# Kernel optimization log

Hardware: AMD Instinct MI355X
Metric: run time of the kernel (lower is better)

The kernel has to match this reference:

```python
import jax, jax.numpy as jnp
import numpy as np

B, S = 16, 1024
V, D, P = 100000, 256, 8


def setup_inputs() -> dict:
    key = jax.random.key(0)
    k1, k2, k3, k4 = jax.random.split(key, 4)
    x = jax.random.randint(k1, (B, S), 0, V, dtype=jnp.int64 if jax.config.jax_enable_x64 else jnp.int32)
    emb_table = jax.random.normal(k2, (V, D), dtype=jnp.float32)
    weight = jax.random.normal(k3, (P, D, D), dtype=jnp.float32)
    partitions = jax.random.randint(k4, (V,), 0, P, dtype=jnp.int32)
    return {"x": x, "emb_table": emb_table, "weight": weight, "partitions": partitions}


def reference(x, emb_table, weight, partitions):
    P_, Dz, Dx = weight.shape
    # mask[p, x] = 1 for x < D >> p (reset_parameters halves active dim per partition)
    active = (Dx >> jnp.arange(P_))  # [P]
    mask = (jnp.arange(Dx)[None, :] < active[:, None]).astype(weight.dtype)  # [P, Dx]
    mw = weight * mask[:, None, :]  # [P, Dz, Dx], masked partition weights

    emb = emb_table[x]          # [B, S, Dx] token embeddings
    part = partitions[x]        # [B, S] partition id per token

    # Compute all P candidate outputs (small fixed P), then select per token.
    # Mathematically identical to gathering mw[part] and doing per-token matvec,
    # but avoids the huge [B,S,Dz,Dx] gathered-weight intermediate.
    all_out = jnp.einsum('bsx,pzx->bspz', emb, mw)  # [B, S, P, Dz]
    out = jnp.take_along_axis(all_out, part[..., None, None], axis=2)[..., 0, :]  # [B, S, Dz]
    return out
```

## Files before the change

kernel.cpp:

```cpp
#include <hip/hip_runtime.h>

__global__ void bucket_k(const int* __restrict__ x, const int* __restrict__ parts,
                         int* __restrict__ counts, int* __restrict__ buckets, int NT) {
    __shared__ int lcount[8];
    __shared__ int lbase[8];
    const int tid = threadIdx.x;
    if (tid < 8) lcount[tid] = 0;
    __syncthreads();

    const int i = blockIdx.x * blockDim.x + tid;
    int p = 0, lpos = 0;
    const bool valid = (i < NT);
    if (valid) {
        p = parts[x[i]];
        lpos = atomicAdd(&lcount[p], 1);
    }
    __syncthreads();
    if (tid < 8)
        lbase[tid] = lcount[tid] ? atomicAdd(&counts[tid], lcount[tid]) : 0;
    __syncthreads();
    if (valid)
        buckets[(size_t)p * NT + lbase[p] + lpos] = i;
}

#define KC 32
#define XB 32

__global__ __launch_bounds__(256)
void fge_gemm(const int* __restrict__ x,
              const float* __restrict__ emb,
              const float* __restrict__ weight,
              const int* __restrict__ counts,
              const int* __restrict__ buckets,
              float* __restrict__ out, int NT) {
    const int p = blockIdx.z;
    const int n = counts[p];
    if ((int)(blockIdx.x * 64) >= n) return;
    const int z0  = blockIdx.y * 64;
    const int K   = 256 >> p;
    const int tid = threadIdx.x;

    __shared__ __align__(16) float w_lds[256][64];
    __shared__ __align__(16) float e_lds[KC][64];
    __shared__ int vrow[64];
    __shared__ int oidx[64];

    {
        const int Kpad = (K < KC) ? KC : K;
        const int wrow = tid >> 2;
        const float* wbase = weight + ((size_t)p * 256 + (z0 + wrow)) * 256;
        for (int colb = (tid & 3) * 4; colb < Kpad; colb += 16) {
            float4 v = *(const float4*)(wbase + colb);
            float vv[4] = {v.x, v.y, v.z, v.w};
#pragma unroll
            for (int c = 0; c < 4; ++c)
                w_lds[colb + c][wrow] = (colb + c < K) ? vv[c] : 0.f;
        }
    }

    const int tz  = tid & 15;
    const int tt  = tid >> 4;
    const int t_l = tid & 63;
    const int xh  = tid >> 6;
    const int nch = (K + KC - 1) / KC;

    for (int t0 = blockIdx.x * 64; t0 < n; t0 += XB * 64) {
        const int ntile = min(64, n - t0);

        __syncthreads();
        if (tid < 64) {
            int idx = 0, row = 0;
            if (t_l < ntile) {
                idx = buckets[(size_t)p * NT + t0 + t_l];
                row = x[idx];
            }
            oidx[t_l] = idx;
            vrow[t_l] = row;
        }
        __syncthreads();

        float acc[4][4] = {};

        for (int ch = 0; ch < nch; ++ch) {
            {
                const bool tv = (t_l < ntile);
                const float* er = emb + (size_t)vrow[t_l] * 256;
                const int gxb = ch * KC + xh * 8;
                float4 a = *(const float4*)(er + gxb);
                float4 b = *(const float4*)(er + gxb + 4);
                float va[8] = {a.x, a.y, a.z, a.w, b.x, b.y, b.z, b.w};
#pragma unroll
                for (int c = 0; c < 8; ++c) {
                    int gx = gxb + c;
                    e_lds[xh * 8 + c][t_l] = (tv && gx < K) ? va[c] : 0.f;
                }
            }
            __syncthreads();

#pragma unroll
            for (int c = 0; c < KC; ++c) {
                const float4 ev = *(const float4*)&e_lds[c][tt * 4];
                const float4 wv = *(const float4*)&w_lds[ch * KC + c][tz * 4];
                const float ea[4] = {ev.x, ev.y, ev.z, ev.w};
                const float wa[4] = {wv.x, wv.y, wv.z, wv.w};
#pragma unroll
                for (int i = 0; i < 4; ++i)
#pragma unroll
                    for (int j = 0; j < 4; ++j)
                        acc[i][j] = fmaf(ea[i], wa[j], acc[i][j]);
            }
            __syncthreads();
        }

#pragma unroll
        for (int i = 0; i < 4; ++i) {
            const int t = tt * 4 + i;
            if (t < ntile) {
                float4 o = {acc[i][0], acc[i][1], acc[i][2], acc[i][3]};
                *(float4*)(out + (size_t)oidx[t] * 256 + z0 + tz * 4) = o;
            }
        }
    }
}

__global__ void naive_k(const int* __restrict__ x, const float* __restrict__ emb,
                        const float* __restrict__ w, const int* __restrict__ parts,
                        float* __restrict__ out, int D, int P) {
    const int i = blockIdx.x;
    const int tokrow = x[i];
    const int p = parts[tokrow];
    const int K = D >> p;
    const float* er = emb + (size_t)tokrow * D;
    for (int z = threadIdx.x; z < D; z += blockDim.x) {
        const float* wr = w + ((size_t)p * D + z) * D;
        float acc = 0.f;
        for (int k = 0; k < K; ++k) acc = fmaf(er[k], wr[k], acc);
        out[(size_t)i * D + z] = acc;
    }
}

extern "C" void kernel_launch(void* const* d_in, const int* in_sizes, int n_in,
                              void* d_out, int out_size, void* d_ws, size_t ws_size,
                              hipStream_t stream) {
    const int*   xi    = (const int*)d_in[0];
    const float* emb   = (const float*)d_in[1];
    const float* wgt   = (const float*)d_in[2];
    const int*   parts = (const int*)d_in[3];
    float* out = (float*)d_out;

    const int NT = in_sizes[0];
    const long long V = in_sizes[3];
    const int D = (int)(in_sizes[1] / V);
    const int P = (int)(in_sizes[2] / ((long long)D * D));
    const size_t need = 32 + (size_t)P * (size_t)NT * sizeof(int);

    if (D == 256 && P == 8 && ws_size >= need) {
        int* counts  = (int*)d_ws;
        int* buckets = (int*)((char*)d_ws + 32);
        hipMemsetAsync(counts, 0, 32, stream);
        bucket_k<<<(NT + 255) / 256, 256, 0, stream>>>(xi, parts, counts, buckets, NT);
        dim3 grid(XB, 4, 8);
        fge_gemm<<<grid, 256, 0, stream>>>(xi, emb, wgt, counts, buckets, out, NT);
    } else {
        naive_k<<<NT, 256, 0, stream>>>(xi, emb, wgt, parts, out, D, P);
    }
}
```

Before: 162.6 us.

## Fuse partition bucketing into GEMM with per-block local token compaction

Removes the separate bucketing kernel, the memset and the global bucket workspace. Each block now scans a fixed range of 384 tokens, keeps those belonging to its partition in shared-memory lists, and runs the tiled matvec on them. This cuts two launches and a global scatter pass. The cost is that every block rescans x and parts for its range, and the grid grows to 43×4×8 blocks that each load a weight slab of up to 64 KB even when they hold only about 48 tokens.

```diff
diff --git a/kernel.cpp b/kernel.cpp
--- a/kernel.cpp
+++ b/kernel.cpp
@@ -1,49 +1,40 @@
 #include <hip/hip_runtime.h>
 
-__global__ void bucket_k(const int* __restrict__ x, const int* __restrict__ parts,
-                         int* __restrict__ counts, int* __restrict__ buckets, int NT) {
-    __shared__ int lcount[8];
-    __shared__ int lbase[8];
-    const int tid = threadIdx.x;
-    if (tid < 8) lcount[tid] = 0;
-    __syncthreads();
-
-    const int i = blockIdx.x * blockDim.x + tid;
-    int p = 0, lpos = 0;
-    const bool valid = (i < NT);
-    if (valid) {
-        p = parts[x[i]];
-        lpos = atomicAdd(&lcount[p], 1);
-    }
-    __syncthreads();
-    if (tid < 8)
-        lbase[tid] = lcount[tid] ? atomicAdd(&counts[tid], lcount[tid]) : 0;
-    __syncthreads();
-    if (valid)
-        buckets[(size_t)p * NT + lbase[p] + lpos] = i;
-}
-
 #define KC 32
-#define XB 32
+#define RANGE 384
 
 __global__ __launch_bounds__(256)
-void fge_gemm(const int* __restrict__ x,
-              const float* __restrict__ emb,
-              const float* __restrict__ weight,
-              const int* __restrict__ counts,
-              const int* __restrict__ buckets,
-              float* __restrict__ out, int NT) {
-    const int p = blockIdx.z;
-    const int n = counts[p];
-    if ((int)(blockIdx.x * 64) >= n) return;
+void fge_fused(const int* __restrict__ x,
+               const float* __restrict__ emb,
+               const float* __restrict__ weight,
+               const int* __restrict__ parts,
+               float* __restrict__ out, int NT) {
+    const int p   = blockIdx.z;
     const int z0  = blockIdx.y * 64;
+    const int s0  = blockIdx.x * RANGE;
+    if (s0 >= NT) return;
+    const int r   = min(RANGE, NT - s0);
     const int K   = 256 >> p;
     const int tid = threadIdx.x;
 
     __shared__ __align__(16) float w_lds[256][64];
     __shared__ __align__(16) float e_lds[KC][64];
-    __shared__ int vrow[64];
-    __shared__ int oidx[64];
+    __shared__ int toklist[RANGE];
+    __shared__ int rowlist[RANGE];
+    __shared__ int nloc;
+
+    if (tid == 0) nloc = 0;
+    __syncthreads();
+
+    for (int t = tid; t < r; t += 256) {
+        const int i   = s0 + t;
+        const int row = x[i];
+        if (parts[row] == p) {
+            const int pos = atomicAdd(&nloc, 1);
+            toklist[pos] = i;
+            rowlist[pos] = row;
+        }
+    }
 
     {
         const int Kpad = (K < KC) ? KC : K;
@@ -57,6 +48,10 @@
                 w_lds[colb + c][wrow] = (colb + c < K) ? vv[c] : 0.f;
         }
     }
+    __syncthreads();
+
+    const int n = nloc;
+    if (n == 0) return;
 
     const int tz  = tid & 15;
     const int tt  = tid >> 4;
@@ -64,27 +59,15 @@
     const int xh  = tid >> 6;
     const int nch = (K + KC - 1) / KC;
 
-    for (int t0 = blockIdx.x * 64; t0 < n; t0 += XB * 64) {
+    for (int t0 = 0; t0 < n; t0 += 64) {
         const int ntile = min(64, n - t0);
-
-        __syncthreads();
-        if (tid < 64) {
-            int idx = 0, row = 0;
-            if (t_l < ntile) {
-                idx = buckets[(size_t)p * NT + t0 + t_l];
-                row = x[idx];
-            }
-            oidx[t_l] = idx;
-            vrow[t_l] = row;
-        }
-        __syncthreads();
-
         float acc[4][4] = {};
 
         for (int ch = 0; ch < nch; ++ch) {
             {
-                const bool tv = (t_l < ntile);
-                const float* er = emb + (size_t)vrow[t_l] * 256;
+                const bool tv  = (t_l < ntile);
+                const int  row = tv ? rowlist[t0 + t_l] : rowlist[0];
+                const float* er = emb + (size_t)row * 256;
                 const int gxb = ch * KC + xh * 8;
                 float4 a = *(const float4*)(er + gxb);
                 float4 b = *(const float4*)(er + gxb + 4);
@@ -117,7 +100,7 @@
             const int t = tt * 4 + i;
             if (t < ntile) {
                 float4 o = {acc[i][0], acc[i][1], acc[i][2], acc[i][3]};
-                *(float4*)(out + (size_t)oidx[t] * 256 + z0 + tz * 4) = o;
+                *(float4*)(out + (size_t)toklist[t0 + t] * 256 + z0 + tz * 4) = o;
             }
         }
     }
@@ -152,15 +135,11 @@
     const long long V = in_sizes[3];
     const int D = (int)(in_sizes[1] / V);
     const int P = (int)(in_sizes[2] / ((long long)D * D));
-    const size_t need = 32 + (size_t)P * (size_t)NT * sizeof(int);
 
-    if (D == 256 && P == 8 && ws_size >= need) {
-        int* counts  = (int*)d_ws;
-        int* buckets = (int*)((char*)d_ws + 32);
-        hipMemsetAsync(counts, 0, 32, stream);
-        bucket_k<<<(NT + 255) / 256, 256, 0, stream>>>(xi, parts, counts, buckets, NT);
-        dim3 grid(XB, 4, 8);
-        fge_gemm<<<grid, 256, 0, stream>>>(xi, emb, wgt, counts, buckets, out, NT);
+    if (D == 256 && P == 8) {
+        const int NR = (NT + RANGE - 1) / RANGE;
+        dim3 grid(NR, 4, 8);
+        fge_fused<<<grid, 256, 0, stream>>>(xi, emb, wgt, parts, out, NT);
     } else {
         naive_k<<<NT, 256, 0, stream>>>(xi, emb, wgt, parts, out, D, P);
     }
```

Measured after the change: 173.0 us. 6.4% more time.

## Replace global atomic bucketing with per-block segments and in-kernel prefix scan

Applied to the files above, without the earlier changes.

The bucketing kernel now writes each block's token indices into a fixed per-block, per-partition segment and records per-block counts, so it no longer needs global atomics or the memset launch. The GEMM kernel computes a prefix sum over the per-block counts in shared memory and finds each token's segment with a binary search. This removes one launch and the global atomic traffic, at the cost of extra scan and search work in every GEMM block and a limit of NB<=64.

```diff
diff --git a/kernel.cpp b/kernel.cpp
--- a/kernel.cpp
+++ b/kernel.cpp
@@ -1,26 +1,22 @@
 #include <hip/hip_runtime.h>
 
-__global__ void bucket_k(const int* __restrict__ x, const int* __restrict__ parts,
-                         int* __restrict__ counts, int* __restrict__ buckets, int NT) {
-    __shared__ int lcount[8];
-    __shared__ int lbase[8];
+__global__ void bucket_seg(const int* __restrict__ x, const int* __restrict__ parts,
+                           int* __restrict__ cnt, int* __restrict__ segs,
+                           int NT, int NB) {
+    __shared__ int lcnt[8];
     const int tid = threadIdx.x;
-    if (tid < 8) lcount[tid] = 0;
+    const int b = blockIdx.x;
+    if (tid < 8) lcnt[tid] = 0;
     __syncthreads();
-
-    const int i = blockIdx.x * blockDim.x + tid;
-    int p = 0, lpos = 0;
-    const bool valid = (i < NT);
-    if (valid) {
-        p = parts[x[i]];
-        lpos = atomicAdd(&lcount[p], 1);
+    const int i = b * 256 + tid;
+    if (i < NT) {
+        const int row = x[i];
+        const int p = parts[row];
+        const int pos = atomicAdd(&lcnt[p], 1);
+        segs[((size_t)p * NB + b) * 256 + pos] = i;
     }
     __syncthreads();
-    if (tid < 8)
-        lbase[tid] = lcount[tid] ? atomicAdd(&counts[tid], lcount[tid]) : 0;
-    __syncthreads();
-    if (valid)
-        buckets[(size_t)p * NT + lbase[p] + lpos] = i;
+    if (tid < 8) cnt[tid * NB + b] = lcnt[tid];
 }
 
 #define KC 32
@@ -30,20 +26,37 @@
 void fge_gemm(const int* __restrict__ x,
               const float* __restrict__ emb,
               const float* __restrict__ weight,
-              const int* __restrict__ counts,
-              const int* __restrict__ buckets,
-              float* __restrict__ out, int NT) {
-    const int p = blockIdx.z;
-    const int n = counts[p];
-    if ((int)(blockIdx.x * 64) >= n) return;
+              const int* __restrict__ cnt,
+              const int* __restrict__ segs,
+              float* __restrict__ out, int NB) {
+    const int p   = blockIdx.z;
     const int z0  = blockIdx.y * 64;
     const int K   = 256 >> p;
     const int tid = threadIdx.x;
 
     __shared__ __align__(16) float w_lds[256][64];
     __shared__ __align__(16) float e_lds[KC][64];
+    __shared__ int pfx[65];
     __shared__ int vrow[64];
     __shared__ int oidx[64];
+
+    {
+        __shared__ int ctmp[64];
+        if (tid < 64) ctmp[tid] = (tid < NB) ? cnt[p * NB + tid] : 0;
+        __syncthreads();
+        for (int d = 1; d < 64; d <<= 1) {
+            int v = 0;
+            if (tid < 64) v = ctmp[tid] + ((tid >= d) ? ctmp[tid - d] : 0);
+            __syncthreads();
+            if (tid < 64) ctmp[tid] = v;
+            __syncthreads();
+        }
+        if (tid < 64) pfx[tid + 1] = ctmp[tid];
+        if (tid == 0) pfx[0] = 0;
+        __syncthreads();
+    }
+    const int n = pfx[64];
+    if ((int)(blockIdx.x * 64) >= n) return;
 
     {
         const int Kpad = (K < KC) ? KC : K;
@@ -71,7 +84,13 @@
         if (tid < 64) {
             int idx = 0, row = 0;
             if (t_l < ntile) {
-                idx = buckets[(size_t)p * NT + t0 + t_l];
+                const int s = t0 + t_l;
+                int b = 0;
+#pragma unroll
+                for (int st = 32; st; st >>= 1)
+                    if (pfx[b + st] <= s) b += st;
+                const int off = s - pfx[b];
+                idx = segs[((size_t)p * NB + b) * 256 + off];
                 row = x[idx];
             }
             oidx[t_l] = idx;
@@ -87,8 +106,8 @@
                 const float* er = emb + (size_t)vrow[t_l] * 256;
                 const int gxb = ch * KC + xh * 8;
                 float4 a = *(const float4*)(er + gxb);
-                float4 b = *(const float4*)(er + gxb + 4);
-                float va[8] = {a.x, a.y, a.z, a.w, b.x, b.y, b.z, b.w};
+                float4 b4 = *(const float4*)(er + gxb + 4);
+                float va[8] = {a.x, a.y, a.z, a.w, b4.x, b4.y, b4.z, b4.w};
 #pragma unroll
                 for (int c = 0; c < 8; ++c) {
                     int gx = gxb + c;
@@ -152,15 +171,17 @@
     const long long V = in_sizes[3];
     const int D = (int)(in_sizes[1] / V);
     const int P = (int)(in_sizes[2] / ((long long)D * D));
-    const size_t need = 32 + (size_t)P * (size_t)NT * sizeof(int);
 
-    if (D == 256 && P == 8 && ws_size >= need) {
-        int* counts  = (int*)d_ws;
-        int* buckets = (int*)((char*)d_ws + 32);
-        hipMemsetAsync(counts, 0, 32, stream);
-        bucket_k<<<(NT + 255) / 256, 256, 0, stream>>>(xi, parts, counts, buckets, NT);
+    const int NB = (NT + 255) / 256;
+    const size_t need = (size_t)8 * NB * 4
+                      + (size_t)8 * NB * 256 * 4;
+
+    if (D == 256 && P == 8 && NB <= 64 && ws_size >= need) {
+        int* cnt  = (int*)d_ws;
+        int* segs = (int*)((char*)d_ws + (size_t)8 * NB * 4);
+        bucket_seg<<<NB, 256, 0, stream>>>(xi, parts, cnt, segs, NT, NB);
         dim3 grid(XB, 4, 8);
-        fge_gemm<<<grid, 256, 0, stream>>>(xi, emb, wgt, counts, buckets, out, NT);
+        fge_gemm<<<grid, 256, 0, stream>>>(xi, emb, wgt, cnt, segs, out, NB);
     } else {
         naive_k<<<NT, 256, 0, stream>>>(xi, emb, wgt, parts, out, D, P);
     }
```

After: 163.5 us. About the same (+0.6%).
